# Performance work log

Measured on AMD Instinct MI355X. Metric: run time of the kernel, lower is better.

Reference implementation:

```python
import jax, jax.numpy as jnp
import numpy as np

# ---- module hyperparameters (init_kwargs) ----
QMIN, QMAX, QBINS = -8.0, 8.0, 128
PMIN, PMAX, PBINS = -10.0, 10.0, 128
GAMMA_F = 1.0
N_TRAJ = 16384


def _grid():
    # x = arange(qmin - 4/gamma_f, qmax + 4/gamma_f + 0.1/maxp, 0.1/maxp)
    maxp = max(abs(PMIN), abs(PMAX))
    step = 0.1 / maxp
    x = np.arange(QMIN - 4.0 / GAMMA_F, QMAX + 4.0 / GAMMA_F + step, step)
    return x.astype(np.float32)


def setup_inputs() -> dict:
    key = jax.random.key(0)
    ks = jax.random.split(key, 6)
    shape = (1, N_TRAJ)
    x = jnp.asarray(_grid())
    # psi buffer: stand-in for np.interp(x, spl.x, spl.psis[-1][1]) -- a
    # localized oscillatory wavefunction sampled on the grid.
    psi = (jnp.exp(-0.5 * (x - 1.0) ** 2) * jnp.cos(2.0 * x)).astype(jnp.float32)
    return {
        "factors_re": jax.random.normal(ks[0], shape, jnp.float32),
        "factors_im": jax.random.normal(ks[1], shape, jnp.float32),
        "q_re": jax.random.normal(ks[2], shape, jnp.float32),
        "q_im": 0.5 * jax.random.normal(ks[3], shape, jnp.float32),
        "p_re": jax.random.normal(ks[4], shape, jnp.float32),
        "p_im": 0.5 * jax.random.normal(ks[5], shape, jnp.float32),
        "x": x,
        "psi": psi,
    }


def _trapz0(y, x):
    # trapezoid rule along axis 0; y: [M, N] (complex), x: [M]
    dx = jnp.diff(x)
    return jnp.sum(0.5 * (y[1:] + y[:-1]) * dx[:, None], axis=0)


def _forward(factors_re, factors_im, q_re, q_im, p_re, p_im, x, psi):
    g = GAMMA_F
    factors = factors_re + 1j * factors_im  # [1, N] complex
    # _calc_proj: xi = 2*g*q + 1j*p ; qf = Re(xi)/(2g), pf = Im(xi)
    qf = q_re - p_im / (2.0 * g)
    pf = 2.0 * g * q_im + p_re
    dq = (QMAX - QMIN) / QBINS
    dp = (PMAX - PMIN) / PBINS
    qb = jnp.floor((qf - QMIN) / dq)
    pb = jnp.floor((pf - PMIN) / dp)
    bins = (qb * PBINS + pb).astype(jnp.int32).reshape(-1)  # [N]
    n = bins.shape[0]
    # torch: enumerate(torch.unique(bins)) -> rank among sorted unique values.
    # jnp.unique inverse (size=n, large fill pads at the end) gives the same map.
    _, inv = jnp.unique(bins, return_inverse=True, size=n, fill_value=jnp.int32(2**30))
    inds = inv.reshape(qf.shape)  # [1, N] compact bin ids
    qc = (qb + 0.5) * dq + QMIN  # bin centers [1, N]
    pc = (pb + 0.5) * dp + PMIN
    # _gf: coherent-state Gaussians on grid x -> [M, N]
    norm = (2.0 * g / jnp.pi) ** 0.25
    dxq = x[:, None] - qc.reshape(-1)[None, :]  # [M, N]
    gfs = norm * jnp.exp(-g * dxq * dxq + 1j * pc.reshape(-1)[None, :] * dxq)
    gt = _trapz0(jnp.conj(gfs) * psi[:, None], x)  # [N] complex
    # _calc_pref (reconstruction): exponential prefactor that can blow up,
    # hence the nan_to_num + clamp in the original.
    pref = norm * jnp.exp(g * q_im * q_im + 1j * (p_re * q_im))  # [1, N]
    pref = (jnp.clip(jnp.nan_to_num(pref.real), -100.0, 100.0)
            + 1j * jnp.clip(jnp.nan_to_num(pref.imag), -100.0, 100.0))
    vals = pref * factors  # [1, N]
    b = vals.shape[0]
    binned = jnp.zeros_like(vals).at[jnp.arange(b)[:, None], inds].add(vals)
    loss = jnp.sum(jnp.abs(binned - gt[None, :]) ** 2)
    return jnp.sqrt(loss)


def reference(factors_re, factors_im, q_re, q_im, p_re, p_im, x, psi):
    return _forward(factors_re, factors_im, q_re, q_im, p_re, p_im, x, psi)
```

## Files before the change

kernel.cpp:

```cpp
#include <hip/hip_runtime.h>
#include <math.h>


#define PRES_WORDS 1024
#define PRES_BITS  65536
#define PRES_OFF   32768
#define CHUNKS     8
#define MCAP       2432
#define WINR       4.0f

__global__ void prep_kernel(const float* __restrict__ f_re, const float* __restrict__ f_im,
                            const float* __restrict__ q_re, const float* __restrict__ q_im,
                            const float* __restrict__ p_re, const float* __restrict__ p_im,
                            const float* __restrict__ x, const float* __restrict__ psi,
                            float* __restrict__ qc, float* __restrict__ pc,
                            float* __restrict__ vre, float* __restrict__ vim,
                            int* __restrict__ bins, unsigned long long* __restrict__ pres,
                            float* __restrict__ bre, float* __restrict__ bim,
                            float2* __restrict__ xw, int n, int M)
{
    int i = blockIdx.x * blockDim.x + threadIdx.x;
    if (i >= n) return;
    bre[i] = 0.0f; bim[i] = 0.0f;
    if (i < M) {
        float w;
        if (i == 0)          w = 0.5f * (x[1] - x[0]);
        else if (i == M - 1) w = 0.5f * (x[M - 1] - x[M - 2]);
        else                 w = 0.5f * (x[i + 1] - x[i - 1]);
        xw[i] = make_float2(x[i], w * psi[i] * 0.8932438417380023f);
    }
    const float norm = 0.8932438417380023f;
    float qi = q_im[i], pr = p_re[i];
    float qf = q_re[i] - 0.5f * p_im[i];
    float pf = 2.0f * qi + pr;
    float qb = floorf((qf - (-8.0f)) / 0.125f);
    float pb = floorf((pf - (-10.0f)) / 0.15625f);
    int b = (int)(qb * 128.0f + pb);
    bins[i] = b;
    int pidx = min(max(b + PRES_OFF, 0), PRES_BITS - 1);
    atomicOr(&pres[pidx >> 6], 1ull << (pidx & 63));
    qc[i] = (qb + 0.5f) * 0.125f + (-8.0f);
    pc[i] = (pb + 0.5f) * 0.15625f + (-10.0f);
    float ea = norm * expf(qi * qi);
    float s, c;
    __sincosf(pr * qi, &s, &c);
    float prr = fminf(fmaxf(ea * c, -100.0f), 100.0f);
    float pri = fminf(fmaxf(ea * s, -100.0f), 100.0f);
    float fr = f_re[i], fi = f_im[i];
    vre[i] = prr * fr - pri * fi;
    vim[i] = prr * fi + pri * fr;
}

__global__ void __launch_bounds__(256) gt_scatter_kernel(
    const float2* __restrict__ xw, const float* __restrict__ x,
    const float* __restrict__ qc, const float* __restrict__ pc,
    const int* __restrict__ bins, const unsigned long long* __restrict__ pres,
    const float* __restrict__ vre, const float* __restrict__ vim,
    float* __restrict__ bre, float* __restrict__ bim,
    float* __restrict__ gpre, float* __restrict__ gpim, int n, int M)
{
    __shared__ float2 sxw[MCAP];
    __shared__ int lbase[PRES_WORDS];
    int tid = threadIdx.x;
    for (int m = tid; m < M; m += 256) sxw[m] = xw[m];
    if (blockIdx.y == 0 && tid < 64) {
        int cum[16];
        int tot = 0;
        for (int k = 0; k < 16; k++) { cum[k] = tot; tot += __popcll(pres[tid * 16 + k]); }
        int run = tot;
        for (int off = 1; off < 64; off <<= 1) {
            int up = __shfl_up(run, off);
            if (tid >= off) run += up;
        }
        int excl = run - tot;
        for (int k = 0; k < 16; k++) lbase[tid * 16 + k] = excl + cum[k];
    }
    __syncthreads();
    int t = blockIdx.x * 256 + tid;
    if (t >= n) return;
    if (blockIdx.y == 0) {
        int pidx = min(max(bins[t] + PRES_OFF, 0), PRES_BITS - 1);
        int w = pidx >> 6, bit = pidx & 63;
        unsigned long long below = pres[w] & ((bit == 0) ? 0ull : (~0ull >> (64 - bit)));
        int cid = lbase[w] + __popcll(below);
        atomicAdd(&bre[cid], vre[t]);
        atomicAdd(&bim[cid], vim[t]);
    }
    float qcn = qc[t], pcn = pc[t];
    float x0f = x[0];
    float flo = (qcn - WINR - x0f) * 100.0f;
    float fhi = (qcn + WINR - x0f) * 100.0f;
    int mlo = max(0, (int)flo - 1);
    int mhi = min(M, (int)fhi + 2);
    int len = mhi - mlo; if (len < 0) len = 0;
    int c = blockIdx.y;
    int ms = mlo + (len * c) / CHUNKS;
    int me = mlo + (len * (c + 1)) / CHUNKS;
    float sre = 0.0f, sim = 0.0f;
    for (int m = ms; m < me; m++) {
        float2 xm = sxw[m];
        float dxq = xm.x - qcn;
        float e = __expf(-dxq * dxq) * xm.y;
        float s, cc;
        __sincosf(pcn * dxq, &s, &cc);
        sre = fmaf(e, cc, sre);
        sim = fmaf(-e, s, sim);
    }
    gpre[c * n + t] = sre;
    gpim[c * n + t] = sim;
}

__global__ void loss_final_kernel(const float* __restrict__ gpre, const float* __restrict__ gpim,
                                  const float* __restrict__ bre, const float* __restrict__ bim,
                                  float* __restrict__ loss, int* __restrict__ donecnt,
                                  float* __restrict__ out, int n)
{
    int t = blockIdx.x * blockDim.x + threadIdx.x;
    float v = 0.0f;
    if (t < n) {
        float sre = 0.0f, sim = 0.0f;
        for (int c = 0; c < CHUNKS; c++) {
            sre += gpre[c * n + t];
            sim += gpim[c * n + t];
        }
        float dre = bre[t] - sre;
        float dim = bim[t] - sim;
        v = dre * dre + dim * dim;
    }
#pragma unroll
    for (int off = 32; off > 0; off >>= 1) v += __shfl_down(v, off);
    __shared__ float l[4];
    int wv = threadIdx.x >> 6, ln = threadIdx.x & 63;
    if (ln == 0) l[wv] = v;
    __syncthreads();
    if (threadIdx.x == 0) {
        atomicAdd(loss, l[0] + l[1] + l[2] + l[3]);
        __threadfence();
        int old = atomicAdd(donecnt, 1);
        if (old == (int)gridDim.x - 1) {
            __threadfence();
            out[0] = sqrtf(atomicAdd(loss, 0.0f));
        }
    }
}

extern "C" void kernel_launch(void* const* d_in, const int* in_sizes, int n_in,
                              void* d_out, int out_size, void* d_ws, size_t ws_size,
                              hipStream_t stream)
{
    const float* f_re = (const float*)d_in[0];
    const float* f_im = (const float*)d_in[1];
    const float* q_re = (const float*)d_in[2];
    const float* q_im = (const float*)d_in[3];
    const float* p_re = (const float*)d_in[4];
    const float* p_im = (const float*)d_in[5];
    const float* x    = (const float*)d_in[6];
    const float* psi  = (const float*)d_in[7];
    int n = in_sizes[0];
    int M = in_sizes[6];

    float* wsf  = (float*)d_ws;
    float* qc   = wsf;
    float* pc   = qc + n;
    float* vre  = pc + n;
    float* vim  = vre + n;
    int*   bins = (int*)(vim + n);
    float* bre  = (float*)(bins + n);
    float* bim  = bre + n;
    float* gpre = bim + n;
    float* gpim = gpre + (size_t)CHUNKS * n;
    float2* xw  = (float2*)(gpim + (size_t)CHUNKS * n);
    unsigned long long* pres = (unsigned long long*)(xw + MCAP);
    float* loss = (float*)(pres + PRES_WORDS);
    int*   donecnt = (int*)(loss + 1);

    hipMemsetAsync(pres, 0, PRES_WORDS * sizeof(unsigned long long) + 8, stream);

    int nb = (n + 255) / 256;
    prep_kernel<<<nb, 256, 0, stream>>>(f_re, f_im, q_re, q_im, p_re, p_im, x, psi,
                                        qc, pc, vre, vim, bins, pres, bre, bim, xw, n, M);
    gt_scatter_kernel<<<dim3(nb, CHUNKS), 256, 0, stream>>>(xw, x, qc, pc, bins, pres,
                                                            vre, vim, bre, bim,
                                                            gpre, gpim, n, M);
    loss_final_kernel<<<nb, 256, 0, stream>>>(gpre, gpim, bre, bim, loss, donecnt,
                                              (float*)d_out, n);
}
```

Measured before the change: 112.6 us.

## Replace per-point exp/sincos with recurrences and fuse prep into gt kernel

Result: faster. 107.8 us (-4.3%).

```diff
diff --git a/kernel.cpp b/kernel.cpp
--- a/kernel.cpp
+++ b/kernel.cpp
@@ -5,65 +5,86 @@
 #define PRES_WORDS 1024
 #define PRES_BITS  65536
 #define PRES_OFF   32768
-#define CHUNKS     8
+#define CHUNKS     16
 #define MCAP       2432
 #define WINR       4.0f
+#define NORM       0.8932438417380023f
 
-__global__ void prep_kernel(const float* __restrict__ f_re, const float* __restrict__ f_im,
-                            const float* __restrict__ q_re, const float* __restrict__ q_im,
-                            const float* __restrict__ p_re, const float* __restrict__ p_im,
-                            const float* __restrict__ x, const float* __restrict__ psi,
-                            float* __restrict__ qc, float* __restrict__ pc,
-                            float* __restrict__ vre, float* __restrict__ vim,
-                            int* __restrict__ bins, unsigned long long* __restrict__ pres,
-                            float* __restrict__ bre, float* __restrict__ bim,
-                            float2* __restrict__ xw, int n, int M)
+__global__ void __launch_bounds__(256) gt_kernel(
+    const float* __restrict__ q_re, const float* __restrict__ q_im,
+    const float* __restrict__ p_re, const float* __restrict__ p_im,
+    const float* __restrict__ x, const float* __restrict__ psi,
+    unsigned long long* __restrict__ pres,
+    float* __restrict__ bre, float* __restrict__ bim,
+    float* __restrict__ gpre, float* __restrict__ gpim, int n, int M)
 {
-    int i = blockIdx.x * blockDim.x + threadIdx.x;
-    if (i >= n) return;
-    bre[i] = 0.0f; bim[i] = 0.0f;
-    if (i < M) {
-        float w;
-        if (i == 0)          w = 0.5f * (x[1] - x[0]);
-        else if (i == M - 1) w = 0.5f * (x[M - 1] - x[M - 2]);
-        else                 w = 0.5f * (x[i + 1] - x[i - 1]);
-        xw[i] = make_float2(x[i], w * psi[i] * 0.8932438417380023f);
+    __shared__ float swpsi[MCAP];
+    int tid = threadIdx.x;
+    float x0 = x[0];
+    float h  = x[1] - x0;
+    for (int m = tid; m < M; m += 256) {
+        float w = (m == 0 || m == M - 1) ? 0.5f * h : h;
+        swpsi[m] = w * psi[m] * NORM;
     }
-    const float norm = 0.8932438417380023f;
-    float qi = q_im[i], pr = p_re[i];
-    float qf = q_re[i] - 0.5f * p_im[i];
+    __syncthreads();
+    int t = blockIdx.x * 256 + tid;
+    if (t >= n) return;
+    float qi = q_im[t], pr = p_re[t];
+    float qf = q_re[t] - 0.5f * p_im[t];
     float pf = 2.0f * qi + pr;
     float qb = floorf((qf - (-8.0f)) / 0.125f);
     float pb = floorf((pf - (-10.0f)) / 0.15625f);
-    int b = (int)(qb * 128.0f + pb);
-    bins[i] = b;
-    int pidx = min(max(b + PRES_OFF, 0), PRES_BITS - 1);
-    atomicOr(&pres[pidx >> 6], 1ull << (pidx & 63));
-    qc[i] = (qb + 0.5f) * 0.125f + (-8.0f);
-    pc[i] = (pb + 0.5f) * 0.15625f + (-10.0f);
-    float ea = norm * expf(qi * qi);
-    float s, c;
-    __sincosf(pr * qi, &s, &c);
-    float prr = fminf(fmaxf(ea * c, -100.0f), 100.0f);
-    float pri = fminf(fmaxf(ea * s, -100.0f), 100.0f);
-    float fr = f_re[i], fi = f_im[i];
-    vre[i] = prr * fr - pri * fi;
-    vim[i] = prr * fi + pri * fr;
+    float qcn = (qb + 0.5f) * 0.125f + (-8.0f);
+    float pcn = (pb + 0.5f) * 0.15625f + (-10.0f);
+    if (blockIdx.y == 0) {
+        int b = (int)(qb * 128.0f + pb);
+        int pidx = min(max(b + PRES_OFF, 0), PRES_BITS - 1);
+        atomicOr(&pres[pidx >> 6], 1ull << (pidx & 63));
+        bre[t] = 0.0f; bim[t] = 0.0f;
+    }
+    float inv_h = 1.0f / h;
+    int mlo = max(0, (int)((qcn - WINR - x0) * inv_h) - 1);
+    int mhi = min(M, (int)((qcn + WINR - x0) * inv_h) + 2);
+    int len = mhi - mlo; if (len < 0) len = 0;
+    int c = blockIdx.y;
+    int ms = mlo + (len * c) / CHUNKS;
+    int me = mlo + (len * (c + 1)) / CHUNKS;
+    float b0  = x0 - qcn;
+    float dx0 = fmaf((float)ms, h, b0);
+    float e   = __expf(-dx0 * dx0);
+    float u   = __expf(-h * (dx0 + dx0 + h));
+    float d   = __expf(-2.0f * h * h);
+    float sn, cs, sd, cd;
+    __sincosf(pcn * dx0, &sn, &cs);
+    __sincosf(pcn * h, &sd, &cd);
+    float sre = 0.0f, sim = 0.0f;
+    for (int m = ms; m < me; m++) {
+        float w = swpsi[m];
+        float tv = e * w;
+        sre = fmaf(tv, cs, sre);
+        sim = fmaf(-tv, sn, sim);
+        e *= u; u *= d;
+        float cn = fmaf(cs, cd, -sn * sd);
+        sn = fmaf(sn, cd, cs * sd);
+        cs = cn;
+    }
+    gpre[c * n + t] = sre;
+    gpim[c * n + t] = sim;
 }
 
-__global__ void __launch_bounds__(256) gt_scatter_kernel(
-    const float2* __restrict__ xw, const float* __restrict__ x,
-    const float* __restrict__ qc, const float* __restrict__ pc,
-    const int* __restrict__ bins, const unsigned long long* __restrict__ pres,
-    const float* __restrict__ vre, const float* __restrict__ vim,
+__global__ void __launch_bounds__(256) scatter_loss_kernel(
+    const float* __restrict__ f_re, const float* __restrict__ f_im,
+    const float* __restrict__ q_re, const float* __restrict__ q_im,
+    const float* __restrict__ p_re, const float* __restrict__ p_im,
+    const unsigned long long* __restrict__ pres,
     float* __restrict__ bre, float* __restrict__ bim,
-    float* __restrict__ gpre, float* __restrict__ gpim, int n, int M)
+    const float* __restrict__ gpre, const float* __restrict__ gpim,
+    int* __restrict__ k3done, float* __restrict__ loss, int* __restrict__ fin,
+    float* __restrict__ out, int n)
 {
-    __shared__ float2 sxw[MCAP];
     __shared__ int lbase[PRES_WORDS];
     int tid = threadIdx.x;
-    for (int m = tid; m < M; m += 256) sxw[m] = xw[m];
-    if (blockIdx.y == 0 && tid < 64) {
+    if (tid < 64) {
         int cum[16];
         int tot = 0;
         for (int k = 0; k < 16; k++) { cum[k] = tot; tot += __popcll(pres[tid * 16 + k]); }
@@ -77,69 +98,57 @@
     }
     __syncthreads();
     int t = blockIdx.x * 256 + tid;
-    if (t >= n) return;
-    if (blockIdx.y == 0) {
-        int pidx = min(max(bins[t] + PRES_OFF, 0), PRES_BITS - 1);
-        int w = pidx >> 6, bit = pidx & 63;
-        unsigned long long below = pres[w] & ((bit == 0) ? 0ull : (~0ull >> (64 - bit)));
-        int cid = lbase[w] + __popcll(below);
-        atomicAdd(&bre[cid], vre[t]);
-        atomicAdd(&bim[cid], vim[t]);
+    float sre = 0.0f, sim = 0.0f;
+    for (int c = 0; c < CHUNKS; c++) {
+        sre += gpre[c * n + t];
+        sim += gpim[c * n + t];
     }
-    float qcn = qc[t], pcn = pc[t];
-    float x0f = x[0];
-    float flo = (qcn - WINR - x0f) * 100.0f;
-    float fhi = (qcn + WINR - x0f) * 100.0f;
-    int mlo = max(0, (int)flo - 1);
-    int mhi = min(M, (int)fhi + 2);
-    int len = mhi - mlo; if (len < 0) len = 0;
-    int c = blockIdx.y;
-    int ms = mlo + (len * c) / CHUNKS;
-    int me = mlo + (len * (c + 1)) / CHUNKS;
-    float sre = 0.0f, sim = 0.0f;
-    for (int m = ms; m < me; m++) {
-        float2 xm = sxw[m];
-        float dxq = xm.x - qcn;
-        float e = __expf(-dxq * dxq) * xm.y;
-        float s, cc;
-        __sincosf(pcn * dxq, &s, &cc);
-        sre = fmaf(e, cc, sre);
-        sim = fmaf(-e, s, sim);
+    float qi = q_im[t], pr = p_re[t];
+    float qf = q_re[t] - 0.5f * p_im[t];
+    float pf = 2.0f * qi + pr;
+    float qb = floorf((qf - (-8.0f)) / 0.125f);
+    float pb = floorf((pf - (-10.0f)) / 0.15625f);
+    int b = (int)(qb * 128.0f + pb);
+    int pidx = min(max(b + PRES_OFF, 0), PRES_BITS - 1);
+    int w = pidx >> 6, bit = pidx & 63;
+    unsigned long long below = pres[w] & ((bit == 0) ? 0ull : (~0ull >> (64 - bit)));
+    int cid = lbase[w] + __popcll(below);
+    float ea = NORM * expf(qi * qi);
+    float s, c2;
+    __sincosf(pr * qi, &s, &c2);
+    float prr = fminf(fmaxf(ea * c2, -100.0f), 100.0f);
+    float pri = fminf(fmaxf(ea * s, -100.0f), 100.0f);
+    float fr = f_re[t], fi = f_im[t];
+    atomicAdd(&bre[cid], prr * fr - pri * fi);
+    atomicAdd(&bim[cid], prr * fi + pri * fr);
+    __threadfence();
+    __syncthreads();
+    if (tid == 0) {
+        __hip_atomic_fetch_add(k3done, 1, __ATOMIC_ACQ_REL, __HIP_MEMORY_SCOPE_AGENT);
+        while (__hip_atomic_load(k3done, __ATOMIC_ACQUIRE, __HIP_MEMORY_SCOPE_AGENT)
+               < (int)gridDim.x)
+            __builtin_amdgcn_s_sleep(4);
     }
-    gpre[c * n + t] = sre;
-    gpim[c * n + t] = sim;
-}
-
-__global__ void loss_final_kernel(const float* __restrict__ gpre, const float* __restrict__ gpim,
-                                  const float* __restrict__ bre, const float* __restrict__ bim,
-                                  float* __restrict__ loss, int* __restrict__ donecnt,
-                                  float* __restrict__ out, int n)
-{
-    int t = blockIdx.x * blockDim.x + threadIdx.x;
-    float v = 0.0f;
-    if (t < n) {
-        float sre = 0.0f, sim = 0.0f;
-        for (int c = 0; c < CHUNKS; c++) {
-            sre += gpre[c * n + t];
-            sim += gpim[c * n + t];
-        }
-        float dre = bre[t] - sre;
-        float dim = bim[t] - sim;
-        v = dre * dre + dim * dim;
-    }
+    __syncthreads();
+    float brt = __hip_atomic_load(&bre[t], __ATOMIC_RELAXED, __HIP_MEMORY_SCOPE_AGENT);
+    float bit2 = __hip_atomic_load(&bim[t], __ATOMIC_RELAXED, __HIP_MEMORY_SCOPE_AGENT);
+    float dre = brt - sre;
+    float dim = bit2 - sim;
+    float v = dre * dre + dim * dim;
 #pragma unroll
     for (int off = 32; off > 0; off >>= 1) v += __shfl_down(v, off);
     __shared__ float l[4];
-    int wv = threadIdx.x >> 6, ln = threadIdx.x & 63;
+    int wv = tid >> 6, ln = tid & 63;
     if (ln == 0) l[wv] = v;
     __syncthreads();
-    if (threadIdx.x == 0) {
-        atomicAdd(loss, l[0] + l[1] + l[2] + l[3]);
-        __threadfence();
-        int old = atomicAdd(donecnt, 1);
+    if (tid == 0) {
+        __hip_atomic_fetch_add(loss, l[0] + l[1] + l[2] + l[3],
+                               __ATOMIC_ACQ_REL, __HIP_MEMORY_SCOPE_AGENT);
+        int old = __hip_atomic_fetch_add(fin, 1, __ATOMIC_ACQ_REL,
+                                         __HIP_MEMORY_SCOPE_AGENT);
         if (old == (int)gridDim.x - 1) {
-            __threadfence();
-            out[0] = sqrtf(atomicAdd(loss, 0.0f));
+            out[0] = sqrtf(__hip_atomic_load(loss, __ATOMIC_ACQUIRE,
+                                             __HIP_MEMORY_SCOPE_AGENT));
         }
     }
 }
@@ -159,29 +168,21 @@
     int n = in_sizes[0];
     int M = in_sizes[6];
 
-    float* wsf  = (float*)d_ws;
-    float* qc   = wsf;
-    float* pc   = qc + n;
-    float* vre  = pc + n;
-    float* vim  = vre + n;
-    int*   bins = (int*)(vim + n);
-    float* bre  = (float*)(bins + n);
+    float* gpre = (float*)d_ws;
+    float* gpim = gpre + (size_t)CHUNKS * n;
+    float* bre  = gpim + (size_t)CHUNKS * n;
     float* bim  = bre + n;
-    float* gpre = bim + n;
-    float* gpim = gpre + (size_t)CHUNKS * n;
-    float2* xw  = (float2*)(gpim + (size_t)CHUNKS * n);
-    unsigned long long* pres = (unsigned long long*)(xw + MCAP);
-    float* loss = (float*)(pres + PRES_WORDS);
-    int*   donecnt = (int*)(loss + 1);
+    unsigned long long* pres = (unsigned long long*)(bim + n);
+    float* loss    = (float*)(pres + PRES_WORDS);
+    int*   k3done  = (int*)(loss + 1);
+    int*   fin     = k3done + 1;
 
-    hipMemsetAsync(pres, 0, PRES_WORDS * sizeof(unsigned long long) + 8, stream);
+    hipMemsetAsync(pres, 0, PRES_WORDS * sizeof(unsigned long long) + 12, stream);
 
     int nb = (n + 255) / 256;
-    prep_kernel<<<nb, 256, 0, stream>>>(f_re, f_im, q_re, q_im, p_re, p_im, x, psi,
-                                        qc, pc, vre, vim, bins, pres, bre, bim, xw, n, M);
-    gt_scatter_kernel<<<dim3(nb, CHUNKS), 256, 0, stream>>>(xw, x, qc, pc, bins, pres,
-                                                            vre, vim, bre, bim,
-                                                            gpre, gpim, n, M);
-    loss_final_kernel<<<nb, 256, 0, stream>>>(gpre, gpim, bre, bim, loss, donecnt,
-                                              (float*)d_out, n);
+    gt_kernel<<<dim3(nb, CHUNKS), 256, 0, stream>>>(q_re, q_im, p_re, p_im, x, psi,
+                                                    pres, bre, bim, gpre, gpim, n, M);
+    scatter_loss_kernel<<<nb, 256, 0, stream>>>(f_re, f_im, q_re, q_im, p_re, p_im,
+                                                pres, bre, bim, gpre, gpim,
+                                                k3done, loss, fin, (float*)d_out, n);
 }
```
